# Kernel tuning notes

Hardware: AMD Instinct MI355X
Metric: run time of the kernel (lower is better)

Reference implementation:

```python
import jax, jax.numpy as jnp
import numpy as np

B, L, D = 4, 2048, 2048
H, KVH = 16, 4
HD = D // H            # 128
G = H // KVH           # GQA group size
K_SEL = L // 4         # top_k_ratio = 0.25 -> 512
MAX_SEQ = 8192
THETA = 10000.0
SCALE = HD ** -0.5
NEG = -1e9


def _rope_tables(dim, max_len, theta):
    inv = 1.0 / theta ** (jnp.arange(0, dim, 2, dtype=jnp.float32) / dim)  # (dim/2,)
    ang = jnp.arange(max_len, dtype=jnp.float32)[:, None] * inv[None, :]   # (max_len, dim/2)
    return jnp.cos(ang), jnp.sin(ang)


def _apply_rope_pos(x, cos, sin, pos):
    # x: (B, h, K, HD), pos: (B, K) int positions
    c = cos[pos][:, None]  # (B,1,K,HD/2)
    s = sin[pos][:, None]
    x1, x2 = jnp.split(x, 2, axis=-1)
    return jnp.concatenate([x1 * c - x2 * s, x1 * s + x2 * c], axis=-1)


def setup_inputs() -> dict:
    key = jax.random.key(0)
    ks = jax.random.split(key, 8)
    std = 0.02
    x   = jax.random.normal(ks[0], (B, L, D), dtype=jnp.float32)
    Wq  = jax.random.normal(ks[1], (D, D), dtype=jnp.float32) * std
    Wkv = jax.random.normal(ks[2], (D, 2 * KVH * HD), dtype=jnp.float32) * std
    Wo  = jax.random.normal(ks[3], (D, D), dtype=jnp.float32) * std
    W1  = jax.random.normal(ks[4], (D, D // 4), dtype=jnp.float32) * std
    b1  = jnp.zeros((D // 4,), dtype=jnp.float32)
    W2  = jax.random.normal(ks[5], (D // 4, 1), dtype=jnp.float32) * std
    b2  = jnp.zeros((1,), dtype=jnp.float32)
    return {"x": x, "Wq": Wq, "Wkv": Wkv, "Wo": Wo,
            "W1": W1, "b1": b1, "W2": W2, "b2": b2}


def reference(x, Wq, Wkv, Wo, W1, b1, W2, b2):
    Bx, Lx, Dx = x.shape
    # 1. learned per-token importance scores
    imp = (jax.nn.gelu(x @ W1 + b1, approximate=False) @ W2 + b2)[..., 0]  # (B,L)
    # 2. top-k token selection, sorted to keep original order
    _, idx = jax.lax.top_k(imp, K_SEL)
    idx = jnp.sort(idx, axis=-1)                                           # (B,K)
    x_sel = jnp.take_along_axis(x, idx[..., None], axis=1)                 # (B,K,D)
    # 3. fused KV projection on the selected subset (GQA)
    kv = x_sel @ Wkv
    k, v = jnp.split(kv, 2, axis=-1)
    k = k.reshape(Bx, K_SEL, KVH, HD).transpose(0, 2, 1, 3)                # (B,KVH,K,HD)
    v = v.reshape(Bx, K_SEL, KVH, HD).transpose(0, 2, 1, 3)
    # 4. RoPE with original positions for K, contiguous positions for Q
    cos, sin = _rope_tables(HD, MAX_SEQ, THETA)
    k = _apply_rope_pos(k, cos, sin, idx)
    q = (x @ Wq).reshape(Bx, Lx, H, HD).transpose(0, 2, 1, 3)              # (B,H,L,HD)
    qpos = jnp.broadcast_to(jnp.arange(Lx)[None, :], (Bx, Lx))
    q = _apply_rope_pos(q, cos, sin, qpos)
    # 5. GQA head expansion + attention over gathered keys
    k = jnp.repeat(k, G, axis=1)                                           # (B,H,K,HD)
    v = jnp.repeat(v, G, axis=1)
    scores = jnp.einsum('bhld,bhkd->bhlk', q, k) * SCALE                   # (B,H,L,K)
    # causal mask on original key positions
    causal = idx[:, None, None, :] > jnp.arange(Lx)[None, None, :, None]
    scores = jnp.where(causal, NEG, scores)
    attn = jax.nn.softmax(scores, axis=-1)
    # 6. importance soft gating (gradient path into the scorer)
    gate = jax.nn.sigmoid(jnp.take_along_axis(imp, idx, axis=1))           # (B,K)
    attn = attn * gate[:, None, None, :]
    out = jnp.einsum('bhlk,bhkd->bhld', attn, v)                           # (B,H,L,HD)
    out = out.transpose(0, 2, 1, 3).reshape(Bx, Lx, Dx)
    return out @ Wo
```

## Files before the change

### kernel.cpp

```cpp
#include <hip/hip_runtime.h>
#include <math.h>

typedef unsigned short u16;
typedef __attribute__((ext_vector_type(8))) short short8;
typedef __attribute__((ext_vector_type(4))) float f32x4;

__device__ __forceinline__ float bf2f(u16 u) {
  return __uint_as_float(((unsigned)u) << 16);
}
__device__ __forceinline__ u16 f2bf(float f) {
  unsigned u = __float_as_uint(f);
  return (u16)((u + 0x7fffu + ((u >> 16) & 1u)) >> 16);
}

__device__ __forceinline__ void gload_lds16(const u16* g, u16* l) {
  __builtin_amdgcn_global_load_lds((const __attribute__((address_space(1))) unsigned int*)g,
                                   (__attribute__((address_space(3))) unsigned int*)l, 16, 0, 0);
}

__device__ __forceinline__ void stage_tile(const u16* __restrict__ gbase, int ldg,
                                           u16* lds, int w, int lane) {
  #pragma unroll
  for (int i = 0; i < 4; ++i) {
    int c = w * 4 + i;
    const u16* g = gbase + (size_t)(c * 8 + (lane >> 3)) * ldg + (lane & 7) * 8;
    gload_lds16(g, lds + c * 512);
  }
}

__global__ __launch_bounds__(256) void cvt_x_kernel(const float* __restrict__ x,
                                                    u16* __restrict__ xb,
                                                    u16* __restrict__ xlo) {
  size_t base = ((size_t)blockIdx.x * 256 + threadIdx.x) * 8;
  short8 hi, lo;
  #pragma unroll
  for (int i = 0; i < 8; ++i) {
    float v = x[base + i];
    u16 h = f2bf(v);
    hi[i] = (short)h;
    lo[i] = (short)f2bf(v - bf2f(h));
  }
  *(short8*)&xb[base] = hi;
  *(short8*)&xlo[base] = lo;
}

template <bool HILO>
__global__ __launch_bounds__(256) void transpose_cvt(const float* __restrict__ in,
                                                     u16* __restrict__ outH,
                                                     u16* __restrict__ outL,
                                                     int R, int C) {
  __shared__ u16 tH[64][72];
  __shared__ u16 tL[64][72];
  int rb = blockIdx.y * 64, cb = blockIdx.x * 64;
  int t = threadIdx.x;
  #pragma unroll
  for (int i = 0; i < 16; ++i) {
    int r = i * 4 + (t >> 6), c = t & 63;
    float v = in[(size_t)(rb + r) * C + cb + c];
    u16 h = f2bf(v);
    tH[r][c] = h;
    if (HILO) tL[r][c] = f2bf(v - bf2f(h));
  }
  __syncthreads();
  #pragma unroll
  for (int i = 0; i < 16; ++i) {
    int r = i * 4 + (t >> 6), c = t & 63;
    outH[(size_t)(cb + r) * R + rb + c] = tH[c][r];
    if (HILO) outL[(size_t)(cb + r) * R + rb + c] = tL[c][r];
  }
}

__global__ void ropetab_kernel(float* __restrict__ cosT, float* __restrict__ sinT) {
  int pos = blockIdx.x, i = threadIdx.x;
  float e = (float)(2 * i) * (1.0f / 128.0f);
  float inv = powf(10000.0f, -e);
  float ang = (float)pos * inv;
  cosT[pos * 64 + i] = cosf(ang);
  sinT[pos * 64 + i] = sinf(ang);
}

template <bool BF16OUT>
__global__ __launch_bounds__(512, 2) void gemm256(const u16* __restrict__ A,
                                                  const u16* __restrict__ BT,
                                                  float* __restrict__ Cf,
                                                  u16* __restrict__ Cb,
                                                  int M, int N, int K) {
  __shared__ __align__(1024) u16 smem[65536];
  const int bm = blockIdx.x * 256, bn = blockIdx.y * 256;
  const int t = threadIdx.x, lane = t & 63, w = t >> 6;
  const int ll = lane & 15, lh = lane >> 4;
  const int wr = w >> 2, wc = w & 3;
  const int NT = K >> 6;

  const int tt0 = t, tt1 = t + 512;
  const int r0 = tt0 >> 2, r1 = tt1 >> 2;
  const int c0 = (((tt0 & 3) ^ ((tt0 >> 3) & 3)) << 3);
  const int c1 = (((tt1 & 3) ^ ((tt1 >> 3) & 3)) << 3);
  const size_t aoff0 = (size_t)(bm + r0) * K + c0;
  const size_t aoff1 = (size_t)(bm + r1) * K + c1;
  const size_t boff0 = (size_t)(bn + r0) * K + c0;
  const size_t boff1 = (size_t)(bn + r1) * K + c1;

  const int swz = ((lh ^ ((ll >> 1) & 3)) << 3);
  const int arow = (wr * 128 + ll) * 32 + swz;
  const int brow = (wc * 64 + ll) * 32 + swz;

  f32x4 acc[8][4];
  #pragma unroll
  for (int mi = 0; mi < 8; ++mi)
    #pragma unroll
    for (int ni = 0; ni < 4; ++ni) acc[mi][ni] = f32x4{0.f, 0.f, 0.f, 0.f};

  short8 aq[8], bq[2];

#define G_STAGE(base, o0, o1, lds) \
  gload_lds16((base) + (o0), (lds) + w * 512); \
  gload_lds16((base) + (o1), (lds) + 4096 + w * 512)
#define RD_A(Sa, ks) \
  _Pragma("unroll") for (int mi = 0; mi < 8; ++mi) aq[mi] = *(const short8*)&(Sa)[(ks)*8192 + arow + mi * 512]
#define RD_B(Sb, ks, nh) \
  _Pragma("unroll") for (int n2 = 0; n2 < 2; ++n2) bq[n2] = *(const short8*)&(Sb)[(ks)*8192 + brow + ((nh)*2 + n2) * 512]
#define DO_MFMA(nh) \
  __builtin_amdgcn_s_setprio(1); \
  _Pragma("unroll") for (int mi = 0; mi < 8; ++mi) \
    _Pragma("unroll") for (int n2 = 0; n2 < 2; ++n2) \
      acc[mi][(nh)*2 + n2] = __builtin_amdgcn_mfma_f32_16x16x32_bf16(aq[mi], bq[n2], acc[mi][(nh)*2 + n2], 0, 0, 0); \
  __builtin_amdgcn_s_setprio(0)
#define VMW(n) asm volatile("s_waitcnt vmcnt(" #n ")" ::: "memory")

  G_STAGE(A, aoff0, aoff1, smem);
  G_STAGE(BT, boff0, boff1, smem + 16384);
  G_STAGE(A, aoff0 + 32, aoff1 + 32, smem + 8192);
  G_STAGE(BT, boff0 + 32, boff1 + 32, smem + 16384 + 8192);

  for (int kt = 0; kt < NT - 1; ++kt) {
    const int cur = kt & 1;
    u16* Sa = smem + cur * 32768;
    u16* Sb = Sa + 16384;
    u16* Pa = smem + (cur ^ 1) * 32768;
    u16* Pb = Pa + 16384;
    const size_t kg = (size_t)(kt + 1) * 64;
    VMW(4);
    __builtin_amdgcn_s_barrier();
    G_STAGE(A, aoff0 + kg, aoff1 + kg, Pa);
    RD_A(Sa, 0);
    RD_B(Sb, 0, 0);
    DO_MFMA(0);
    G_STAGE(BT, boff0 + kg, boff1 + kg, Pb);
    RD_B(Sb, 0, 1);
    DO_MFMA(1);
    VMW(4);
    __builtin_amdgcn_s_barrier();
    G_STAGE(A, aoff0 + kg + 32, aoff1 + kg + 32, Pa + 8192);
    RD_A(Sa, 1);
    RD_B(Sb, 1, 0);
    DO_MFMA(0);
    G_STAGE(BT, boff0 + kg + 32, boff1 + kg + 32, Pb + 8192);
    RD_B(Sb, 1, 1);
    DO_MFMA(1);
  }
  {
    const int cur = (NT - 1) & 1;
    u16* Sa = smem + cur * 32768;
    u16* Sb = Sa + 16384;
    VMW(4);
    __builtin_amdgcn_s_barrier();
    RD_A(Sa, 0); RD_B(Sb, 0, 0); DO_MFMA(0);
    RD_B(Sb, 0, 1); DO_MFMA(1);
    VMW(0);
    __builtin_amdgcn_s_barrier();
    RD_A(Sa, 1); RD_B(Sb, 1, 0); DO_MFMA(0);
    RD_B(Sb, 1, 1); DO_MFMA(1);
  }

  #pragma unroll
  for (int mi = 0; mi < 8; ++mi)
    #pragma unroll
    for (int ni = 0; ni < 4; ++ni)
      #pragma unroll
      for (int r = 0; r < 4; ++r) {
        int row = bm + wr * 128 + mi * 16 + lh * 4 + r;
        int col = bn + wc * 64 + ni * 16 + ll;
        float v = acc[mi][ni][r];
        if (BF16OUT) Cb[(size_t)row * N + col] = f2bf(v);
        else Cf[(size_t)row * N + col] = v;
      }
#undef G_STAGE
#undef RD_A
#undef RD_B
#undef DO_MFMA
#undef VMW
}

__global__ __launch_bounds__(256) void gemm_bt_gather(const u16* __restrict__ A,
                                                      const u16* __restrict__ BT,
                                                      const int* __restrict__ rowidx,
                                                      u16* __restrict__ Cb,
                                                      int M, int N, int K) {
  constexpr int BK = 64;
  __shared__ u16 As[128][BK + 8];
  __shared__ u16 Bs[128][BK + 8];
  const int bm = blockIdx.x * 128, bn = blockIdx.y * 128;
  const int t = threadIdx.x, lane = t & 63, w = t >> 6;
  const int lh = lane >> 4, ll = lane & 15;
  const int wm = (w >> 1) * 64, wn = (w & 1) * 64;
  f32x4 acc[4][4];
  #pragma unroll
  for (int mt = 0; mt < 4; ++mt)
    #pragma unroll
    for (int nt = 0; nt < 4; ++nt) acc[mt][nt] = f32x4{0.f, 0.f, 0.f, 0.f};

  for (int kb = 0; kb < K; kb += BK) {
    __syncthreads();
    #pragma unroll
    for (int i = 0; i < 4; ++i) {
      int e = t + i * 256;
      int row = e >> 3, c8 = e & 7;
      int arow = rowidx[bm + row];
      *(short8*)&As[row][c8 * 8] = *(const short8*)&A[(size_t)arow * K + kb + c8 * 8];
      *(short8*)&Bs[row][c8 * 8] = *(const short8*)&BT[(size_t)(bn + row) * K + kb + c8 * 8];
    }
    __syncthreads();
    #pragma unroll
    for (int ks = 0; ks < 2; ++ks) {
      short8 a[4], b[4];
      #pragma unroll
      for (int mt = 0; mt < 4; ++mt) a[mt] = *(const short8*)&As[wm + mt * 16 + ll][ks * 32 + lh * 8];
      #pragma unroll
      for (int nt = 0; nt < 4; ++nt) b[nt] = *(const short8*)&Bs[wn + nt * 16 + ll][ks * 32 + lh * 8];
      #pragma unroll
      for (int mt = 0; mt < 4; ++mt)
        #pragma unroll
        for (int nt = 0; nt < 4; ++nt)
          acc[mt][nt] = __builtin_amdgcn_mfma_f32_16x16x32_bf16(a[mt], b[nt], acc[mt][nt], 0, 0, 0);
    }
  }
  #pragma unroll
  for (int mt = 0; mt < 4; ++mt)
    #pragma unroll
    for (int nt = 0; nt < 4; ++nt)
      #pragma unroll
      for (int r = 0; r < 4; ++r) {
        int row = bm + wm + mt * 16 + lh * 4 + r;
        int col = bn + wn + nt * 16 + ll;
        Cb[(size_t)row * N + col] = f2bf(acc[mt][nt][r]);
      }
}

__global__ __launch_bounds__(256) void gemm_scorer(const u16* __restrict__ Ahi,
                                                   const u16* __restrict__ Alo,
                                                   const u16* __restrict__ Bhi,
                                                   const u16* __restrict__ Blo,
                                                   float* __restrict__ Cpart,
                                                   int M, int N, int K) {
  __shared__ __align__(1024) u16 smem[4 * 128 * 64];
  u16* AsH = smem;
  u16* AsL = smem + 128 * 64;
  u16* BsH = smem + 2 * 128 * 64;
  u16* BsL = smem + 3 * 128 * 64;
  const int bm = blockIdx.x * 128, bn = blockIdx.y * 128;
  const int kz = blockIdx.z;
  const int t = threadIdx.x, lane = t & 63, w = t >> 6;
  const int lh = lane >> 4, ll = lane & 15;
  const int wm = (w >> 1) * 64, wn = (w & 1) * 64;
  f32x4 acc[4][4];
  #pragma unroll
  for (int mt = 0; mt < 4; ++mt)
    #pragma unroll
    for (int nt = 0; nt < 4; ++nt) acc[mt][nt] = f32x4{0.f, 0.f, 0.f, 0.f};

  const int k0 = kz * (K / 2), k1 = k0 + K / 2;
  for (int kb = k0; kb < k1; kb += 64) {
    __syncthreads();
    stage_tile(Ahi + (size_t)bm * K + kb, K, AsH, w, lane);
    stage_tile(Alo + (size_t)bm * K + kb, K, AsL, w, lane);
    stage_tile(Bhi + (size_t)bn * K + kb, K, BsH, w, lane);
    stage_tile(Blo + (size_t)bn * K + kb, K, BsL, w, lane);
    __syncthreads();
    #pragma unroll
    for (int ks = 0; ks < 2; ++ks) {
      short8 ah[4], al[4], bh[4], bl[4];
      #pragma unroll
      for (int mt = 0; mt < 4; ++mt) {
        int o = (wm + mt * 16 + ll) * 64 + ks * 32 + lh * 8;
        ah[mt] = *(const short8*)&AsH[o];
        al[mt] = *(const short8*)&AsL[o];
      }
      #pragma unroll
      for (int nt = 0; nt < 4; ++nt) {
        int o = (wn + nt * 16 + ll) * 64 + ks * 32 + lh * 8;
        bh[nt] = *(const short8*)&BsH[o];
        bl[nt] = *(const short8*)&BsL[o];
      }
      #pragma unroll
      for (int mt = 0; mt < 4; ++mt)
        #pragma unroll
        for (int nt = 0; nt < 4; ++nt) {
          acc[mt][nt] = __builtin_amdgcn_mfma_f32_16x16x32_bf16(ah[mt], bh[nt], acc[mt][nt], 0, 0, 0);
          acc[mt][nt] = __builtin_amdgcn_mfma_f32_16x16x32_bf16(ah[mt], bl[nt], acc[mt][nt], 0, 0, 0);
          acc[mt][nt] = __builtin_amdgcn_mfma_f32_16x16x32_bf16(al[mt], bh[nt], acc[mt][nt], 0, 0, 0);
        }
    }
  }
  float* C = Cpart + (size_t)kz * M * N;
  #pragma unroll
  for (int mt = 0; mt < 4; ++mt)
    #pragma unroll
    for (int nt = 0; nt < 4; ++nt)
      #pragma unroll
      for (int r = 0; r < 4; ++r) {
        int row = bm + wm + mt * 16 + lh * 4 + r;
        int col = bn + wn + nt * 16 + ll;
        C[(size_t)row * N + col] = acc[mt][nt][r];
      }
}

__global__ __launch_bounds__(256) void scorer_finish(const float* __restrict__ hg,
                                                     const float* __restrict__ b1,
                                                     const float* __restrict__ W2,
                                                     const float* __restrict__ b2,
                                                     float* __restrict__ imp) {
  int tok = blockIdx.x * 4 + (threadIdx.x >> 6);
  int lane = threadIdx.x & 63;
  const float* h0 = hg + (size_t)tok * 512;
  const float* h1 = hg + (size_t)8192 * 512 + (size_t)tok * 512;
  float s = 0.f;
  #pragma unroll
  for (int i = 0; i < 8; ++i) {
    int c = lane + i * 64;
    float v = h0[c] + h1[c] + b1[c];
    v = 0.5f * v * (1.0f + erff(v * 0.70710678118654752f));
    s += v * W2[c];
  }
  #pragma unroll
  for (int off = 32; off; off >>= 1) s += __shfl_xor(s, off, 64);
  if (lane == 0) imp[tok] = s + b2[0];
}

__global__ __launch_bounds__(1024) void topk_kernel(const float* __restrict__ imp,
                                                    int* __restrict__ idx_sel,
                                                    int* __restrict__ sel_rows,
                                                    float* __restrict__ gatev) {
  __shared__ float v[2048];
  __shared__ int ix[2048];
  __shared__ int ids[512];
  int b = blockIdx.x, t = threadIdx.x;
  for (int i = t; i < 2048; i += 1024) { v[i] = imp[b * 2048 + i]; ix[i] = i; }
  __syncthreads();
  for (int k = 2; k <= 2048; k <<= 1)
    for (int j = k >> 1; j > 0; j >>= 1) {
      int i = ((t & ~(j - 1)) << 1) | (t & (j - 1));
      int l2 = i | j;
      bool dir = ((i & k) == 0);
      float vi = v[i], vl = v[l2];
      int xi = ix[i], xl = ix[l2];
      bool g = (vi < vl) || (vi == vl && xi > xl);
      if (g == dir) { v[i] = vl; v[l2] = vi; ix[i] = xl; ix[l2] = xi; }
      __syncthreads();
    }
  if (t < 512) ids[t] = ix[t];
  __syncthreads();
  for (int k = 2; k <= 512; k <<= 1)
    for (int j = k >> 1; j > 0; j >>= 1) {
      if (t < 256) {
        int i = ((t & ~(j - 1)) << 1) | (t & (j - 1));
        int l2 = i | j;
        bool dir = ((i & k) == 0);
        int ai = ids[i], al = ids[l2];
        if ((ai > al) == dir) { ids[i] = al; ids[l2] = ai; }
      }
      __syncthreads();
    }
  if (t < 512) {
    int id = ids[t];
    idx_sel[b * 512 + t] = id;
    sel_rows[b * 512 + t] = b * 2048 + id;
    float g = imp[b * 2048 + id];
    gatev[b * 512 + t] = 1.0f / (1.0f + __expf(-g));
  }
}

__global__ __launch_bounds__(256) void rope_q_kernel(u16* __restrict__ q,
                                                     const float* __restrict__ cosT,
                                                     const float* __restrict__ sinT) {
  int gid = blockIdx.x * 256 + threadIdx.x;
  int i = gid & 63, h = (gid >> 6) & 15;
  int tok = gid >> 10;
  int l = tok & 2047;
  size_t base = (size_t)tok * 2048 + h * 128 + i;
  float q1 = bf2f(q[base]), q2 = bf2f(q[base + 64]);
  float c = cosT[l * 64 + i], s = sinT[l * 64 + i];
  q[base] = f2bf(q1 * c - q2 * s);
  q[base + 64] = f2bf(q1 * s + q2 * c);
}

__global__ __launch_bounds__(256) void rope_k_kernel(const u16* __restrict__ kv,
                                                     const int* __restrict__ idx_sel,
                                                     const float* __restrict__ cosT,
                                                     const float* __restrict__ sinT,
                                                     u16* __restrict__ Kb) {
  int gid = blockIdx.x * 256 + threadIdx.x;
  int i = gid & 63;
  int s = (gid >> 6) & 511;
  int kvh = (gid >> 15) & 3;
  int b = gid >> 17;
  size_t src = (size_t)(b * 512 + s) * 1024 + kvh * 128 + i;
  float k1 = bf2f(kv[src]), k2 = bf2f(kv[src + 64]);
  int pos = idx_sel[b * 512 + s];
  float c = cosT[pos * 64 + i], sn = sinT[pos * 64 + i];
  size_t dst = (size_t)((b * 4 + kvh) * 512 + s) * 128 + i;
  Kb[dst] = f2bf(k1 * c - k2 * sn);
  Kb[dst + 64] = f2bf(k1 * sn + k2 * c);
}

__global__ __launch_bounds__(256) void vtrans_kernel(const u16* __restrict__ kv,
                                                     const float* __restrict__ gatev,
                                                     u16* __restrict__ VT) {
  int gid = blockIdx.x * 256 + threadIdx.x;
  int s = gid & 511;
  int d = (gid >> 9) & 127;
  int kvh = (gid >> 16) & 3;
  int b = gid >> 18;
  float v = bf2f(kv[(size_t)(b * 512 + s) * 1024 + 512 + kvh * 128 + d]);
  VT[(size_t)((b * 4 + kvh) * 128 + d) * 512 + s] = f2bf(v * gatev[b * 512 + s]);
}

__global__ __launch_bounds__(512) void attn_kernel(const u16* __restrict__ Qb,
                                                   const u16* __restrict__ Kb,
                                                   const u16* __restrict__ VTb,
                                                   const int* __restrict__ idxp,
                                                   u16* __restrict__ Ob) {
  __shared__ u16 Ks[64][136];
  __shared__ u16 Vs[128][76];
  __shared__ u16 Ps[8][16][76];
  __shared__ int idx_s[64];

  const int qt = blockIdx.x, h = blockIdx.y, b = blockIdx.z;
  const int kvh = h >> 2;
  const int t = threadIdx.x, lane = t & 63, w = t >> 6;
  const int lh = lane >> 4, ll = lane & 15;
  const int q0 = qt * 128;
  const float SCALE_LOG2E = 0.12753102331f;

  int NT = 8;
  if (idxp[b * 512] <= q0) {
    NT = 1;
    while (NT < 8 && idxp[b * 512 + NT * 64] <= q0 + 127) ++NT;
  }

  short8 aq[4];
  #pragma unroll
  for (int ks = 0; ks < 4; ++ks)
    aq[ks] = *(const short8*)&Qb[(size_t)(b * 2048 + q0 + w * 16 + ll) * 2048 + h * 128 + ks * 32 + lh * 8];

  const u16* Kbase = Kb + (size_t)((b * 4 + kvh) * 512) * 128;
  const u16* Vbase = VTb + (size_t)((b * 4 + kvh) * 128) * 512;
  const int krow = t >> 4, kc8 = t & 15;
  const int vrow = t >> 3, vc8 = t & 7;
  short8 kreg0, kreg1, vreg0, vreg1;
  auto load_kv = [&](int kt) {
    kreg0 = *(const short8*)&Kbase[(size_t)(kt * 64 + krow) * 128 + kc8 * 8];
    kreg1 = *(const short8*)&Kbase[(size_t)(kt * 64 + krow + 32) * 128 + kc8 * 8];
    vreg0 = *(const short8*)&Vbase[(size_t)vrow * 512 + kt * 64 + vc8 * 8];
    vreg1 = *(const short8*)&Vbase[(size_t)(vrow + 64) * 512 + kt * 64 + vc8 * 8];
  };
  load_kv(0);

  float m[4], lden[4];
  f32x4 O[8];
  #pragma unroll
  for (int r = 0; r < 4; ++r) { m[r] = -INFINITY; lden[r] = 0.f; }
  #pragma unroll
  for (int dt = 0; dt < 8; ++dt) O[dt] = f32x4{0.f, 0.f, 0.f, 0.f};

  for (int kt = 0; kt < NT; ++kt) {
    const int tmax = idxp[b * 512 + kt * 64 + 63];
    const bool nomask = (tmax <= q0 + w * 16);

    __syncthreads();
    *(short8*)&Ks[krow][kc8 * 8] = kreg0;
    *(short8*)&Ks[krow + 32][kc8 * 8] = kreg1;
    *(short8*)&Vs[vrow][vc8 * 8] = vreg0;
    *(short8*)&Vs[vrow + 64][vc8 * 8] = vreg1;
    if (t < 64) idx_s[t] = idxp[b * 512 + kt * 64 + t];
    __syncthreads();
    if (kt + 1 < NT) load_kv(kt + 1);

    f32x4 S[4];
    #pragma unroll
    for (int nt = 0; nt < 4; ++nt) S[nt] = f32x4{0.f, 0.f, 0.f, 0.f};
    #pragma unroll
    for (int nt = 0; nt < 4; ++nt)
      #pragma unroll
      for (int ks = 0; ks < 4; ++ks) {
        short8 bk = *(const short8*)&Ks[nt * 16 + ll][ks * 32 + lh * 8];
        S[nt] = __builtin_amdgcn_mfma_f32_16x16x32_bf16(aq[ks], bk, S[nt], 0, 0, 0);
      }

    float p[4][4], lmax[4];
    #pragma unroll
    for (int r = 0; r < 4; ++r) lmax[r] = -INFINITY;
    if (nomask) {
      #pragma unroll
      for (int nt = 0; nt < 4; ++nt)
        #pragma unroll
        for (int r = 0; r < 4; ++r) {
          float s = S[nt][r] * SCALE_LOG2E;
          p[nt][r] = s;
          lmax[r] = fmaxf(lmax[r], s);
        }
    } else {
      #pragma unroll
      for (int nt = 0; nt < 4; ++nt) {
        int kpos = idx_s[nt * 16 + ll];
        #pragma unroll
        for (int r = 0; r < 4; ++r) {
          int row = q0 + w * 16 + lh * 4 + r;
          float s = S[nt][r] * SCALE_LOG2E;
          if (kpos > row) s = -1e9f;
          p[nt][r] = s;
          lmax[r] = fmaxf(lmax[r], s);
        }
      }
    }
    #pragma unroll
    for (int off = 8; off; off >>= 1)
      #pragma unroll
      for (int r = 0; r < 4; ++r) lmax[r] = fmaxf(lmax[r], __shfl_xor(lmax[r], off, 64));

    bool need = false;
    #pragma unroll
    for (int r = 0; r < 4; ++r) need = need || (lmax[r] > m[r] + 8.0f);
    if (__any(need)) {
      #pragma unroll
      for (int r = 0; r < 4; ++r) {
        float mnew = fmaxf(m[r], lmax[r]);
        float alpha = exp2f(m[r] - mnew);
        m[r] = mnew;
        lden[r] *= alpha;
        #pragma unroll
        for (int dt = 0; dt < 8; ++dt) O[dt][r] *= alpha;
      }
    }

    float rs[4] = {0.f, 0.f, 0.f, 0.f};
    #pragma unroll
    for (int nt = 0; nt < 4; ++nt)
      #pragma unroll
      for (int r = 0; r < 4; ++r) {
        float e = exp2f(p[nt][r] - m[r]);
        p[nt][r] = e;
        rs[r] += e;
      }
    #pragma unroll
    for (int off = 8; off; off >>= 1)
      #pragma unroll
      for (int r = 0; r < 4; ++r) rs[r] += __shfl_xor(rs[r], off, 64);
    #pragma unroll
    for (int r = 0; r < 4; ++r) lden[r] += rs[r];

    #pragma unroll
    for (int nt = 0; nt < 4; ++nt)
      #pragma unroll
      for (int r = 0; r < 4; r += 2) {
        unsigned pk;
        asm("v_cvt_pk_bf16_f32 %0, %1, %2" : "=v"(pk) : "v"(p[nt][r]), "v"(p[nt][r + 1]));
        Ps[w][lh * 4 + r][nt * 16 + ll] = (u16)pk;
        Ps[w][lh * 4 + r + 1][nt * 16 + ll] = (u16)(pk >> 16);
      }
    #pragma unroll
    for (int ks = 0; ks < 2; ++ks) {
      short8 pa = *(const short8*)&Ps[w][ll][ks * 32 + lh * 8];
      #pragma unroll
      for (int dt = 0; dt < 8; ++dt) {
        short8 vb = *(const short8*)&Vs[dt * 16 + ll][ks * 32 + lh * 8];
        O[dt] = __builtin_amdgcn_mfma_f32_16x16x32_bf16(pa, vb, O[dt], 0, 0, 0);
      }
    }
  }

  #pragma unroll
  for (int dt = 0; dt < 8; ++dt)
    #pragma unroll
    for (int r = 0; r < 4; ++r) {
      int row = q0 + w * 16 + lh * 4 + r;
      int col = h * 128 + dt * 16 + ll;
      Ob[(size_t)(b * 2048 + row) * 2048 + col] = f2bf(O[dt][r] / lden[r]);
    }
}

extern "C" void kernel_launch(void* const* d_in, const int* in_sizes, int n_in,
                              void* d_out, int out_size, void* d_ws, size_t ws_size,
                              hipStream_t stream) {
  const float* x = (const float*)d_in[0];
  const float* Wq = (const float*)d_in[1];
  const float* Wkv = (const float*)d_in[2];
  const float* Wo = (const float*)d_in[3];
  const float* W1 = (const float*)d_in[4];
  const float* b1 = (const float*)d_in[5];
  const float* W2 = (const float*)d_in[6];
  const float* b2 = (const float*)d_in[7];
  float* out = (float*)d_out;

  char* ws = (char*)d_ws;
  size_t off = 0;
  auto alloc = [&](size_t bytes) {
    char* p = ws + off;
    off = (off + bytes + 255) & ~(size_t)255;
    return p;
  };
  u16* xb = (u16*)alloc((size_t)8192 * 2048 * 2);
  u16* xlo = (u16*)alloc((size_t)8192 * 2048 * 2);
  u16* W1Th = (u16*)alloc((size_t)512 * 2048 * 2);
  u16* W1Tl = (u16*)alloc((size_t)512 * 2048 * 2);
  u16* WqT = (u16*)alloc((size_t)2048 * 2048 * 2);
  u16* WkvT = (u16*)alloc((size_t)1024 * 2048 * 2);
  u16* WoT = (u16*)alloc((size_t)2048 * 2048 * 2);
  float* cosT = (float*)alloc((size_t)2048 * 64 * 4);
  float* sinT = (float*)alloc((size_t)2048 * 64 * 4);
  float* hg = (float*)alloc((size_t)2 * 8192 * 512 * 4);
  float* impv = (float*)alloc((size_t)8192 * 4);
  int* idx_sel = (int*)alloc((size_t)2048 * 4);
  int* sel_rows = (int*)alloc((size_t)2048 * 4);
  float* gatev = (float*)alloc((size_t)2048 * 4);
  u16* qbuf = (u16*)alloc((size_t)8192 * 2048 * 2);
  u16* kvbuf = (u16*)alloc((size_t)2048 * 1024 * 2);
  u16* Kbuf = (u16*)alloc((size_t)4 * 4 * 512 * 128 * 2);
  u16* VTbuf = (u16*)alloc((size_t)4 * 4 * 128 * 512 * 2);
  u16* attn_out = xlo;

  cvt_x_kernel<<<8192, 256, 0, stream>>>(x, xb, xlo);
  transpose_cvt<true><<<dim3(512 / 64, 2048 / 64), 256, 0, stream>>>(W1, W1Th, W1Tl, 2048, 512);
  transpose_cvt<false><<<dim3(32, 32), 256, 0, stream>>>(Wq, WqT, nullptr, 2048, 2048);
  transpose_cvt<false><<<dim3(16, 32), 256, 0, stream>>>(Wkv, WkvT, nullptr, 2048, 1024);
  transpose_cvt<false><<<dim3(32, 32), 256, 0, stream>>>(Wo, WoT, nullptr, 2048, 2048);
  ropetab_kernel<<<2048, 64, 0, stream>>>(cosT, sinT);

  gemm_scorer<<<dim3(64, 4, 2), 256, 0, stream>>>(xb, xlo, W1Th, W1Tl, hg, 8192, 512, 2048);
  scorer_finish<<<2048, 256, 0, stream>>>(hg, b1, W2, b2, impv);
  topk_kernel<<<4, 1024, 0, stream>>>(impv, idx_sel, sel_rows, gatev);

  gemm256<true><<<dim3(32, 8), 512, 0, stream>>>(xb, WqT, nullptr, qbuf, 8192, 2048, 2048);
  rope_q_kernel<<<32768, 256, 0, stream>>>(qbuf, cosT, sinT);

  gemm_bt_gather<<<dim3(16, 8), 256, 0, stream>>>(xb, WkvT, sel_rows, kvbuf, 2048, 1024, 2048);
  rope_k_kernel<<<2048, 256, 0, stream>>>(kvbuf, idx_sel, cosT, sinT, Kbuf);
  vtrans_kernel<<<4096, 256, 0, stream>>>(kvbuf, gatev, VTbuf);

  attn_kernel<<<dim3(16, 16, 4), 512, 0, stream>>>(qbuf, Kbuf, VTbuf, idx_sel, attn_out);

  gemm256<false><<<dim3(32, 8), 512, 0, stream>>>(attn_out, WoT, out, nullptr, 8192, 2048, 2048);
}
```

Before: 413.7 us.

## Fuse Q RoPE into attention, split-K KV gather GEMM, shrink attention LDS

Removes the standalone rope_q kernel and applies Q RoPE inside the attention kernel right after Q is loaded into registers. The gathered KV GEMM is split along K into two fp32 partials (doubling the grid), and the rope_k/vtrans kernels sum those partials. The attention kernel merges its K and P shared buffers, drops the register prefetch of the next K/V tile and reads idx from global memory, with a launch-bounds hint for higher occupancy. The trade-off is an extra sync per tile, less load/compute overlap, and more fp32 partial traffic.

```diff
diff --git a/kernel.cpp b/kernel.cpp
--- a/kernel.cpp
+++ b/kernel.cpp
@@ -195,12 +195,13 @@
 __global__ __launch_bounds__(256) void gemm_bt_gather(const u16* __restrict__ A,
                                                       const u16* __restrict__ BT,
                                                       const int* __restrict__ rowidx,
-                                                      u16* __restrict__ Cb,
+                                                      float* __restrict__ Cpart,
                                                       int M, int N, int K) {
   constexpr int BK = 64;
   __shared__ u16 As[128][BK + 8];
   __shared__ u16 Bs[128][BK + 8];
   const int bm = blockIdx.x * 128, bn = blockIdx.y * 128;
+  const int kz = blockIdx.z;
   const int t = threadIdx.x, lane = t & 63, w = t >> 6;
   const int lh = lane >> 4, ll = lane & 15;
   const int wm = (w >> 1) * 64, wn = (w & 1) * 64;
@@ -210,7 +211,8 @@
     #pragma unroll
     for (int nt = 0; nt < 4; ++nt) acc[mt][nt] = f32x4{0.f, 0.f, 0.f, 0.f};
 
-  for (int kb = 0; kb < K; kb += BK) {
+  const int k0 = kz * (K / 2), k1 = k0 + K / 2;
+  for (int kb = k0; kb < k1; kb += BK) {
     __syncthreads();
     #pragma unroll
     for (int i = 0; i < 4; ++i) {
@@ -235,6 +237,7 @@
           acc[mt][nt] = __builtin_amdgcn_mfma_f32_16x16x32_bf16(a[mt], b[nt], acc[mt][nt], 0, 0, 0);
     }
   }
+  float* C = Cpart + (size_t)kz * M * N;
   #pragma unroll
   for (int mt = 0; mt < 4; ++mt)
     #pragma unroll
@@ -243,7 +246,7 @@
       for (int r = 0; r < 4; ++r) {
         int row = bm + wm + mt * 16 + lh * 4 + r;
         int col = bn + wn + nt * 16 + ll;
-        Cb[(size_t)row * N + col] = f2bf(acc[mt][nt][r]);
+        C[(size_t)row * N + col] = acc[mt][nt][r];
       }
 }
 
@@ -380,32 +383,19 @@
   }
 }
 
-__global__ __launch_bounds__(256) void rope_q_kernel(u16* __restrict__ q,
-                                                     const float* __restrict__ cosT,
-                                                     const float* __restrict__ sinT) {
-  int gid = blockIdx.x * 256 + threadIdx.x;
-  int i = gid & 63, h = (gid >> 6) & 15;
-  int tok = gid >> 10;
-  int l = tok & 2047;
-  size_t base = (size_t)tok * 2048 + h * 128 + i;
-  float q1 = bf2f(q[base]), q2 = bf2f(q[base + 64]);
-  float c = cosT[l * 64 + i], s = sinT[l * 64 + i];
-  q[base] = f2bf(q1 * c - q2 * s);
-  q[base + 64] = f2bf(q1 * s + q2 * c);
-}
-
-__global__ __launch_bounds__(256) void rope_k_kernel(const u16* __restrict__ kv,
-                                                     const int* __restrict__ idx_sel,
-                                                     const float* __restrict__ cosT,
-                                                     const float* __restrict__ sinT,
-                                                     u16* __restrict__ Kb) {
+__global__ __launch_bounds__(256) void rope_k2(const float* __restrict__ part,
+                                               const int* __restrict__ idx_sel,
+                                               const float* __restrict__ cosT,
+                                               const float* __restrict__ sinT,
+                                               u16* __restrict__ Kb) {
   int gid = blockIdx.x * 256 + threadIdx.x;
   int i = gid & 63;
   int s = (gid >> 6) & 511;
   int kvh = (gid >> 15) & 3;
   int b = gid >> 17;
   size_t src = (size_t)(b * 512 + s) * 1024 + kvh * 128 + i;
-  float k1 = bf2f(kv[src]), k2 = bf2f(kv[src + 64]);
+  float k1 = part[src] + part[src + 2097152];
+  float k2 = part[src + 64] + part[src + 64 + 2097152];
   int pos = idx_sel[b * 512 + s];
   float c = cosT[pos * 64 + i], sn = sinT[pos * 64 + i];
   size_t dst = (size_t)((b * 4 + kvh) * 512 + s) * 128 + i;
@@ -413,27 +403,28 @@
   Kb[dst + 64] = f2bf(k1 * sn + k2 * c);
 }
 
-__global__ __launch_bounds__(256) void vtrans_kernel(const u16* __restrict__ kv,
-                                                     const float* __restrict__ gatev,
-                                                     u16* __restrict__ VT) {
+__global__ __launch_bounds__(256) void vtrans2(const float* __restrict__ part,
+                                               const float* __restrict__ gatev,
+                                               u16* __restrict__ VT) {
   int gid = blockIdx.x * 256 + threadIdx.x;
   int s = gid & 511;
   int d = (gid >> 9) & 127;
   int kvh = (gid >> 16) & 3;
   int b = gid >> 18;
-  float v = bf2f(kv[(size_t)(b * 512 + s) * 1024 + 512 + kvh * 128 + d]);
+  size_t src = (size_t)(b * 512 + s) * 1024 + 512 + kvh * 128 + d;
+  float v = part[src] + part[src + 2097152];
   VT[(size_t)((b * 4 + kvh) * 128 + d) * 512 + s] = f2bf(v * gatev[b * 512 + s]);
 }
 
-__global__ __launch_bounds__(512) void attn_kernel(const u16* __restrict__ Qb,
-                                                   const u16* __restrict__ Kb,
-                                                   const u16* __restrict__ VTb,
-                                                   const int* __restrict__ idxp,
-                                                   u16* __restrict__ Ob) {
-  __shared__ u16 Ks[64][136];
+__global__ __launch_bounds__(512, 8) void attn_kernel(const u16* __restrict__ Qb,
+                                                      const u16* __restrict__ Kb,
+                                                      const u16* __restrict__ VTb,
+                                                      const int* __restrict__ idxp,
+                                                      const float* __restrict__ cosT,
+                                                      const float* __restrict__ sinT,
+                                                      u16* __restrict__ Ob) {
+  __shared__ u16 KPs[8704];
   __shared__ u16 Vs[128][76];
-  __shared__ u16 Ps[8][16][76];
-  __shared__ int idx_s[64];
 
   const int qt = blockIdx.x, h = blockIdx.y, b = blockIdx.z;
   const int kvh = h >> 2;
@@ -448,43 +439,53 @@
     while (NT < 8 && idxp[b * 512 + NT * 64] <= q0 + 127) ++NT;
   }
 
+  const int lrow = q0 + w * 16 + ll;
   short8 aq[4];
   #pragma unroll
   for (int ks = 0; ks < 4; ++ks)
-    aq[ks] = *(const short8*)&Qb[(size_t)(b * 2048 + q0 + w * 16 + ll) * 2048 + h * 128 + ks * 32 + lh * 8];
-
-  const u16* Kbase = Kb + (size_t)((b * 4 + kvh) * 512) * 128;
-  const u16* Vbase = VTb + (size_t)((b * 4 + kvh) * 128) * 512;
+    aq[ks] = *(const short8*)&Qb[(size_t)(b * 2048 + lrow) * 2048 + h * 128 + ks * 32 + lh * 8];
+  {
+    const float* cp = cosT + (size_t)lrow * 64 + lh * 8;
+    const float* sp = sinT + (size_t)lrow * 64 + lh * 8;
+    short8 n0, n1, n2, n3;
+    #pragma unroll
+    for (int j = 0; j < 8; ++j) {
+      float cA = cp[j], sA = sp[j], cB = cp[32 + j], sB = sp[32 + j];
+      float x0 = bf2f((u16)aq[0][j]), x2 = bf2f((u16)aq[2][j]);
+      float x1 = bf2f((u16)aq[1][j]), x3 = bf2f((u16)aq[3][j]);
+      n0[j] = (short)f2bf(x0 * cA - x2 * sA);
+      n2[j] = (short)f2bf(x0 * sA + x2 * cA);
+      n1[j] = (short)f2bf(x1 * cB - x3 * sB);
+      n3[j] = (short)f2bf(x1 * sB + x3 * cB);
+    }
+    aq[0] = n0; aq[1] = n1; aq[2] = n2; aq[3] = n3;
+  }
+
+  float m[4], lden[4];
+  f32x4 O[8];
+  #pragma unroll
+  for (int r = 0; r < 4; ++r) { m[r] = -INFINITY; lden[r] = 0.f; }
+  #pragma unroll
+  for (int dt = 0; dt < 8; ++dt) O[dt] = f32x4{0.f, 0.f, 0.f, 0.f};
+
   const int krow = t >> 4, kc8 = t & 15;
   const int vrow = t >> 3, vc8 = t & 7;
-  short8 kreg0, kreg1, vreg0, vreg1;
-  auto load_kv = [&](int kt) {
-    kreg0 = *(const short8*)&Kbase[(size_t)(kt * 64 + krow) * 128 + kc8 * 8];
-    kreg1 = *(const short8*)&Kbase[(size_t)(kt * 64 + krow + 32) * 128 + kc8 * 8];
-    vreg0 = *(const short8*)&Vbase[(size_t)vrow * 512 + kt * 64 + vc8 * 8];
-    vreg1 = *(const short8*)&Vbase[(size_t)(vrow + 64) * 512 + kt * 64 + vc8 * 8];
-  };
-  load_kv(0);
-
-  float m[4], lden[4];
-  f32x4 O[8];
-  #pragma unroll
-  for (int r = 0; r < 4; ++r) { m[r] = -INFINITY; lden[r] = 0.f; }
-  #pragma unroll
-  for (int dt = 0; dt < 8; ++dt) O[dt] = f32x4{0.f, 0.f, 0.f, 0.f};
 
   for (int kt = 0; kt < NT; ++kt) {
     const int tmax = idxp[b * 512 + kt * 64 + 63];
     const bool nomask = (tmax <= q0 + w * 16);
 
     __syncthreads();
-    *(short8*)&Ks[krow][kc8 * 8] = kreg0;
-    *(short8*)&Ks[krow + 32][kc8 * 8] = kreg1;
-    *(short8*)&Vs[vrow][vc8 * 8] = vreg0;
-    *(short8*)&Vs[vrow + 64][vc8 * 8] = vreg1;
-    if (t < 64) idx_s[t] = idxp[b * 512 + kt * 64 + t];
+    #pragma unroll
+    for (int i = 0; i < 2; ++i) {
+      int kr = krow + i * 32;
+      *(short8*)&KPs[kr * 136 + kc8 * 8] =
+          *(const short8*)&Kb[(size_t)((b * 4 + kvh) * 512 + kt * 64 + kr) * 128 + kc8 * 8];
+      int vr = vrow + i * 64;
+      *(short8*)&Vs[vr][vc8 * 8] =
+          *(const short8*)&VTb[(size_t)((b * 4 + kvh) * 128 + vr) * 512 + kt * 64 + vc8 * 8];
+    }
     __syncthreads();
-    if (kt + 1 < NT) load_kv(kt + 1);
 
     f32x4 S[4];
     #pragma unroll
@@ -493,9 +494,10 @@
     for (int nt = 0; nt < 4; ++nt)
       #pragma unroll
       for (int ks = 0; ks < 4; ++ks) {
-        short8 bk = *(const short8*)&Ks[nt * 16 + ll][ks * 32 + lh * 8];
+        short8 bk = *(const short8*)&KPs[(nt * 16 + ll) * 136 + ks * 32 + lh * 8];
         S[nt] = __builtin_amdgcn_mfma_f32_16x16x32_bf16(aq[ks], bk, S[nt], 0, 0, 0);
       }
+    __syncthreads();
 
     float p[4][4], lmax[4];
     #pragma unroll
@@ -512,7 +514,7 @@
     } else {
       #pragma unroll
       for (int nt = 0; nt < 4; ++nt) {
-        int kpos = idx_s[nt * 16 + ll];
+        int kpos = idxp[b * 512 + kt * 64 + nt * 16 + ll];
         #pragma unroll
         for (int r = 0; r < 4; ++r) {
           int row = q0 + w * 16 + lh * 4 + r;
@@ -565,12 +567,12 @@
       for (int r = 0; r < 4; r += 2) {
         unsigned pk;
         asm("v_cvt_pk_bf16_f32 %0, %1, %2" : "=v"(pk) : "v"(p[nt][r]), "v"(p[nt][r + 1]));
-        Ps[w][lh * 4 + r][nt * 16 + ll] = (u16)pk;
-        Ps[w][lh * 4 + r + 1][nt * 16 + ll] = (u16)(pk >> 16);
+        KPs[w * 1088 + (lh * 4 + r) * 68 + nt * 16 + ll] = (u16)pk;
+        KPs[w * 1088 + (lh * 4 + r + 1) * 68 + nt * 16 + ll] = (u16)(pk >> 16);
       }
     #pragma unroll
     for (int ks = 0; ks < 2; ++ks) {
-      short8 pa = *(const short8*)&Ps[w][ll][ks * 32 + lh * 8];
+      short8 pa = *(const short8*)&KPs[w * 1088 + ll * 68 + ks * 32 + lh * 8];
       #pragma unroll
       for (int dt = 0; dt < 8; ++dt) {
         short8 vb = *(const short8*)&Vs[dt * 16 + ll][ks * 32 + lh * 8];
@@ -624,10 +626,10 @@
   int* sel_rows = (int*)alloc((size_t)2048 * 4);
   float* gatev = (float*)alloc((size_t)2048 * 4);
   u16* qbuf = (u16*)alloc((size_t)8192 * 2048 * 2);
-  u16* kvbuf = (u16*)alloc((size_t)2048 * 1024 * 2);
   u16* Kbuf = (u16*)alloc((size_t)4 * 4 * 512 * 128 * 2);
   u16* VTbuf = (u16*)alloc((size_t)4 * 4 * 128 * 512 * 2);
   u16* attn_out = xlo;
+  float* kvpart = hg;
 
   cvt_x_kernel<<<8192, 256, 0, stream>>>(x, xb, xlo);
   transpose_cvt<true><<<dim3(512 / 64, 2048 / 64), 256, 0, stream>>>(W1, W1Th, W1Tl, 2048, 512);
@@ -641,13 +643,12 @@
   topk_kernel<<<4, 1024, 0, stream>>>(impv, idx_sel, sel_rows, gatev);
 
   gemm256<true><<<dim3(32, 8), 512, 0, stream>>>(xb, WqT, nullptr, qbuf, 8192, 2048, 2048);
-  rope_q_kernel<<<32768, 256, 0, stream>>>(qbuf, cosT, sinT);
-
-  gemm_bt_gather<<<dim3(16, 8), 256, 0, stream>>>(xb, WkvT, sel_rows, kvbuf, 2048, 1024, 2048);
-  rope_k_kernel<<<2048, 256, 0, stream>>>(kvbuf, idx_sel, cosT, sinT, Kbuf);
-  vtrans_kernel<<<4096, 256, 0, stream>>>(kvbuf, gatev, VTbuf);
-
-  attn_kernel<<<dim3(16, 16, 4), 512, 0, stream>>>(qbuf, Kbuf, VTbuf, idx_sel, attn_out);
+
+  gemm_bt_gather<<<dim3(16, 8, 2), 256, 0, stream>>>(xb, WkvT, sel_rows, kvpart, 2048, 1024, 2048);
+  rope_k2<<<2048, 256, 0, stream>>>(kvpart, idx_sel, cosT, sinT, Kbuf);
+  vtrans2<<<4096, 256, 0, stream>>>(kvpart, gatev, VTbuf);
+
+  attn_kernel<<<dim3(16, 16, 4), 512, 0, stream>>>(qbuf, Kbuf, VTbuf, idx_sel, cosT, sinT, attn_out);
 
   gemm256<false><<<dim3(32, 8), 512, 0, stream>>>(attn_out, WoT, out, nullptr, 8192, 2048, 2048);
 }
```

Result: slower. 546.2 us (+32.0%).
